# Performance work log

Hardware: AMD Instinct MI355X
Metric: run time of the kernel (lower is better)

## Reference

```python
import jax, jax.numpy as jnp
import numpy as np

K = 5          # number of spline bins
B = 5.0        # tail bound
HIDDEN = 8
MIN_W = 1e-3; MIN_H = 1e-3; MIN_D = 1e-3  # RQS defaults (Durkan et al.)


def setup_inputs() -> dict:
    n, d = 32768, 64
    L = d - 1
    P = 3 * K - 1
    ks = jax.random.split(jax.random.key(0), 8)
    x = jax.random.normal(ks[0], (n, d), jnp.float32) * 2.0
    init_param = jax.random.uniform(ks[1], (P,), jnp.float32, -0.5, 0.5)
    # ragged first layers: layer l (predicts dim l+1) sees x[:, :l+1]; zero-pad to width L
    mask = (jnp.arange(L)[None, :] <= jnp.arange(L)[:, None]).astype(jnp.float32)
    W1 = jax.random.normal(ks[2], (L, L, HIDDEN), jnp.float32) * 0.2 * mask[:, :, None]
    b1 = jax.random.normal(ks[3], (L, HIDDEN), jnp.float32) * 0.1
    W2 = jax.random.normal(ks[4], (L, HIDDEN, HIDDEN), jnp.float32) * 0.2
    b2 = jax.random.normal(ks[5], (L, HIDDEN), jnp.float32) * 0.1
    W3 = jax.random.normal(ks[6], (L, HIDDEN, P), jnp.float32) * 0.2
    b3 = jax.random.normal(ks[7], (L, P), jnp.float32) * 0.1
    return {"x": x, "init_param": init_param, "W1": W1, "b1": b1,
            "W2": W2, "b2": b2, "W3": W3, "b3": b3}


def _rqs(xf, Wu, Hu, Du):
    # xf: (M,), Wu/Hu: (M,K), Du: (M,K-1) -- vectorized unconstrained RQS, forward
    inside = (xf >= -B) & (xf <= B)
    const = float(np.log(np.exp(1.0 - MIN_D) - 1.0))
    Dpad = jnp.pad(Du, ((0, 0), (1, 1)), constant_values=const)

    widths = MIN_W + (1.0 - MIN_W * K) * jax.nn.softmax(Wu, axis=-1)
    cumw = jnp.pad(jnp.cumsum(widths, -1), ((0, 0), (1, 0)))
    cumw = 2.0 * B * cumw - B
    cumw = cumw.at[:, 0].set(-B).at[:, -1].set(B)
    widths = cumw[:, 1:] - cumw[:, :-1]

    heights = MIN_H + (1.0 - MIN_H * K) * jax.nn.softmax(Hu, axis=-1)
    cumh = jnp.pad(jnp.cumsum(heights, -1), ((0, 0), (1, 0)))
    cumh = 2.0 * B * cumh - B
    cumh = cumh.at[:, 0].set(-B).at[:, -1].set(B)
    heights = cumh[:, 1:] - cumh[:, :-1]

    derivs = MIN_D + jax.nn.softplus(Dpad)  # (M, K+1)

    xc = jnp.clip(xf, -B, B)
    idx = jnp.clip(jnp.sum(xc[:, None] >= cumw, axis=-1) - 1, 0, K - 1)
    take = lambda a: jnp.take_along_axis(a, idx[:, None], axis=-1)[:, 0]

    icw, ibw = take(cumw), take(widths)
    ich, ih = take(cumh), take(heights)
    idl = take(heights / widths)
    idv = take(derivs)
    idvp1 = take(derivs[:, 1:])

    theta = (xc - icw) / ibw
    tmt = theta * (1.0 - theta)
    num = ih * (idl * theta * theta + idv * tmt)
    den = idl + (idv + idvp1 - 2.0 * idl) * tmt
    out = ich + num / den
    dnum = idl * idl * (idvp1 * theta * theta + 2.0 * idl * tmt + idv * (1.0 - theta) ** 2)
    ld = jnp.log(dnum) - 2.0 * jnp.log(den)
    return jnp.where(inside, out, xf), jnp.where(inside, ld, 0.0)


def reference(x, init_param, W1, b1, W2, b2, W3, b3):
    n, d = x.shape
    L = d - 1
    P = 3 * K - 1
    # mask re-applied so padded W1 entries are exactly inert (ragged Linear(i, hidden))
    mask = (jnp.arange(L)[None, :] <= jnp.arange(L)[:, None]).astype(x.dtype)
    h = jnp.tanh(jnp.einsum('nj,ljh->lnh', x[:, :L], W1 * mask[:, :, None]) + b1[:, None, :])
    h = jnp.tanh(jnp.einsum('lnh,lhg->lng', h, W2) + b2[:, None, :])
    out = jnp.einsum('lng,lgp->lnp', h, W3) + b3[:, None, :]      # (L, n, P)
    p0 = jnp.broadcast_to(init_param, (1, n, P))                  # dim 0 uses init_param
    params = jnp.concatenate([p0, out], axis=0).reshape(d * n, P)  # dim-major, matches Ws layout
    Wu, Hu, Du = params[:, :K], params[:, K:2 * K], params[:, 2 * K:]
    xf = x.T.reshape(-1)  # x.transpose(0,1).flatten()
    zs, lds = _rqs(xf, Wu, Hu, Du)
    # NOTE: faithfully replicates the original's reshape of the dim-major flat
    # vector directly to (n, d) (as in the torch source).
    return zs.reshape(n, d), lds.reshape(n, d).sum(axis=1)
```

## Files before the change

### kernel.cpp

```cpp
#include <hip/hip_runtime.h>
#include <hip/hip_bf16.h>
#include <math.h>

#define KK 5
#define Bc 5.0f
#define NN 32768
#define DD 64
#define LL 63
#define PP 14
#define MIN_Wc 0.001f
#define MIN_Hc 0.001f
#define MIN_Dc 0.001f

typedef float f4 __attribute__((ext_vector_type(4)));
typedef float f32x4 __attribute__((ext_vector_type(4)));
typedef float f2 __attribute__((ext_vector_type(2)));
typedef short short8 __attribute__((ext_vector_type(8)));

__device__ __forceinline__ float rcp_fast(float v)  { return __builtin_amdgcn_rcpf(v); }
__device__ __forceinline__ float exp_fast(float v)  { return __expf(v); }
__device__ __forceinline__ float log_fast(float v)  { return __logf(v); }
__device__ __forceinline__ float tanh_fast(float v) {
    float e = exp_fast(2.0f * v);
    return 1.0f - 2.0f * rcp_fast(e + 1.0f);
}
__device__ __forceinline__ float softplus_fast(float v) {
    return (v > 15.0f) ? v : log_fast(1.0f + exp_fast(v));
}
__device__ __forceinline__ ushort to_bf16u(float v) {
    __hip_bfloat16 b = __float2bfloat16(v);
    return *(ushort*)&b;
}
__device__ __forceinline__ f2 splat2(float v) { f2 r; r.x = v; r.y = v; return r; }
__device__ __forceinline__ f4 splat4(float v) { f4 r; r.x = v; r.y = v; r.z = v; r.w = v; return r; }

__global__ __launch_bounds__(256) void pack_b1(const float* __restrict__ W1,
                                               ushort* __restrict__ Bp) {
    int id = blockIdx.x * 256 + threadIdx.x;
    int n = id >> 6, k = id & 63;
    float v = 0.f;
    if (n < 504 && k < 63) {
        int l = n >> 3, h = n & 7;
        v = W1[(l * 63 + k) * 8 + h];
    }
    Bp[id] = to_bf16u(v);
}

__device__ __forceinline__ short8 pack_a(f4 v0, f4 v1) {
    short8 a;
    a[0] = (short)to_bf16u(v0.x); a[1] = (short)to_bf16u(v0.y);
    a[2] = (short)to_bf16u(v0.z); a[3] = (short)to_bf16u(v0.w);
    a[4] = (short)to_bf16u(v1.x); a[5] = (short)to_bf16u(v1.y);
    a[6] = (short)to_bf16u(v1.z); a[7] = (short)to_bf16u(v1.w);
    return a;
}

#define WSL 216

__device__ __forceinline__ void do_dim(
    int dd, const float* wp, float xf, uint4 hv, int s0, int lane, int bx,
    const float* __restrict__ init_param, float* __restrict__ out)
{
    float p0,p1,p2,p3,p4,p5,p6,p7,p8,p9,p10,p11,p12,p13;
    if (dd == 0) {
        p0 = init_param[0];  p1 = init_param[1];  p2 = init_param[2];
        p3 = init_param[3];  p4 = init_param[4];  p5 = init_param[5];
        p6 = init_param[6];  p7 = init_param[7];  p8 = init_param[8];
        p9 = init_param[9];  p10 = init_param[10]; p11 = init_param[11];
        p12 = init_param[12]; p13 = init_param[13];
    } else {
        float h1f[8];
        h1f[0] = __uint_as_float(hv.x << 16);
        h1f[1] = __uint_as_float(hv.x & 0xFFFF0000u);
        h1f[2] = __uint_as_float(hv.y << 16);
        h1f[3] = __uint_as_float(hv.y & 0xFFFF0000u);
        h1f[4] = __uint_as_float(hv.z << 16);
        h1f[5] = __uint_as_float(hv.z & 0xFFFF0000u);
        h1f[6] = __uint_as_float(hv.w << 16);
        h1f[7] = __uint_as_float(hv.w & 0xFFFF0000u);

        f4 h2a = *(const f4*)(wp + 64);
        f4 h2b = *(const f4*)(wp + 68);
        #pragma unroll
        for (int h = 0; h < 8; ++h) {
            f4 wa = *(const f4*)(wp + h * 8);
            f4 wb = *(const f4*)(wp + h * 8 + 4);
            f4 av = splat4(h1f[h]);
            h2a += av * wa;
            h2b += av * wb;
        }
        float h2f[8];
        h2f[0] = tanh_fast(h2a.x); h2f[1] = tanh_fast(h2a.y);
        h2f[2] = tanh_fast(h2a.z); h2f[3] = tanh_fast(h2a.w);
        h2f[4] = tanh_fast(h2b.x); h2f[5] = tanh_fast(h2b.y);
        h2f[6] = tanh_fast(h2b.z); h2f[7] = tanh_fast(h2b.w);

        f4 ppa = *(const f4*)(wp + 200);
        f4 ppb = *(const f4*)(wp + 204);
        f4 ppc = *(const f4*)(wp + 208);
        f4 ppd = *(const f4*)(wp + 212);
        #pragma unroll
        for (int g = 0; g < 8; ++g) {
            const float* wr = wp + 72 + g * 16;
            f4 w0 = *(const f4*)(wr);
            f4 w1 = *(const f4*)(wr + 4);
            f4 w2v = *(const f4*)(wr + 8);
            f4 w3v = *(const f4*)(wr + 12);
            f4 av = splat4(h2f[g]);
            ppa += av * w0;
            ppb += av * w1;
            ppc += av * w2v;
            ppd += av * w3v;
        }
        p0 = ppa.x; p1 = ppa.y; p2 = ppa.z; p3 = ppa.w;
        p4 = ppb.x; p5 = ppb.y; p6 = ppb.z; p7 = ppb.w;
        p8 = ppc.x; p9 = ppc.y; p10 = ppc.z; p11 = ppc.w;
        p12 = ppd.x; p13 = ppd.y;
    }

    f2 e0, e1, e2, e3, e4;
    e0.x = exp_fast(p0); e0.y = exp_fast(p5);
    e1.x = exp_fast(p1); e1.y = exp_fast(p6);
    e2.x = exp_fast(p2); e2.y = exp_fast(p7);
    e3.x = exp_fast(p3); e3.y = exp_fast(p8);
    e4.x = exp_fast(p4); e4.y = exp_fast(p9);
    f2 es = e0 + e1 + e2 + e3 + e4;
    f2 nrm; nrm.x = 0.995f * rcp_fast(es.x); nrm.y = 0.995f * rcp_fast(es.y);

    const f2 minv = {MIN_Wc, MIN_Hc};
    f2 cb0 = splat2(-Bc), acc2 = splat2(0.f);
    acc2 += minv + nrm * e0;  f2 cb1 = splat2(2.f * Bc) * acc2 - splat2(Bc);
    acc2 += minv + nrm * e1;  f2 cb2 = splat2(2.f * Bc) * acc2 - splat2(Bc);
    acc2 += minv + nrm * e2;  f2 cb3 = splat2(2.f * Bc) * acc2 - splat2(Bc);
    acc2 += minv + nrm * e3;  f2 cb4 = splat2(2.f * Bc) * acc2 - splat2(Bc);
    f2 cb5 = splat2(Bc);

    const float xc = fminf(fmaxf(xf, -Bc), Bc);

    float icw = cb0.x, ich = cb0.y;
    float ibw = cb1.x - cb0.x, ih = cb1.y - cb0.y;
    float rv = p10, rvp = p10;
    bool v_one = true, vp_one = false;
    {
        bool c = xc >= cb1.x; f2 dif = cb2 - cb1;
        icw = c ? cb1.x : icw; ich = c ? cb1.y : ich;
        ibw = c ? dif.x : ibw; ih  = c ? dif.y : ih;
        v_one = c ? false : v_one; rv = c ? p10 : rv; rvp = c ? p11 : rvp;
    }
    {
        bool c = xc >= cb2.x; f2 dif = cb3 - cb2;
        icw = c ? cb2.x : icw; ich = c ? cb2.y : ich;
        ibw = c ? dif.x : ibw; ih  = c ? dif.y : ih;
        rv = c ? p11 : rv; rvp = c ? p12 : rvp;
    }
    {
        bool c = xc >= cb3.x; f2 dif = cb4 - cb3;
        icw = c ? cb3.x : icw; ich = c ? cb3.y : ich;
        ibw = c ? dif.x : ibw; ih  = c ? dif.y : ih;
        rv = c ? p12 : rv; rvp = c ? p13 : rvp;
    }
    {
        bool c = xc >= cb4.x; f2 dif = cb5 - cb4;
        icw = c ? cb4.x : icw; ich = c ? cb4.y : ich;
        ibw = c ? dif.x : ibw; ih  = c ? dif.y : ih;
        rv = c ? p13 : rv; vp_one = c;
    }
    const float idv   = v_one  ? 1.0f : MIN_Dc + softplus_fast(rv);
    const float idvp1 = vp_one ? 1.0f : MIN_Dc + softplus_fast(rvp);

    const float ibw_r = rcp_fast(ibw);
    const float idl = ih * ibw_r;
    const float theta = (xc - icw) * ibw_r;
    const float omt = 1.0f - theta;
    const float tmt = theta * omt;
    const float num = ih * (idl * theta * theta + idv * tmt);
    const float den = idl + (idv + idvp1 - 2.0f * idl) * tmt;
    const float dr = rcp_fast(den);
    const float outv = ich + num * dr;
    const float dnum = idl * idl * (idvp1 * theta * theta + 2.0f * idl * tmt + idv * omt * omt);
    const float ld = log_fast(dnum * dr * dr);

    const bool inside = (xf >= -Bc) && (xf <= Bc);
    const float z = inside ? outv : xf;
    float ldv = inside ? ld : 0.0f;

    out[dd * NN + s0 + lane] = z;

    #pragma unroll
    for (int off = 32; off > 0; off >>= 1) ldv += __shfl_down(ldv, off);
    if (lane == 0) out[NN * DD + dd * (NN / 64) + bx] = ldv;
}

#define H1S 136
__global__ __launch_bounds__(256, 5) void fused_kernel(
    const float* __restrict__ x, const float* __restrict__ init_param,
    const ushort* __restrict__ Bp, const float* __restrict__ b1,
    const float* __restrict__ W2, const float* __restrict__ b2,
    const float* __restrict__ W3, const float* __restrict__ b3,
    float* __restrict__ out)
{
    __shared__ ushort h1c[64 * H1S];
    __shared__ float  wl[16 * WSL];
    const int tid = threadIdx.x;
    const int s0 = blockIdx.x * 64;
    const int y  = blockIdx.y;
    const int bx = blockIdx.x;
    const int lane = tid & 63;
    const int wave = __builtin_amdgcn_readfirstlane(tid >> 6);
    const int ln = lane & 15, qg = lane >> 4;
    const int m0 = wave * 16;
    const int l0 = y * 16;

    const float* xrow = x + (size_t)(s0 + lane) * 64;
    const int db = y * 16 + 1 + wave * 4;
    float xv0 = xrow[db];
    float xv1 = xrow[db + 1];
    float xv2 = xrow[db + 2];
    float xv3 = xrow[(y == 3 && wave == 3) ? 0 : db + 3];

    short8 a0, a1;
    {
        const float* xr = x + (size_t)(s0 + m0 + ln) * 64 + qg * 8;
        a0 = pack_a(*(const f4*)xr, *(const f4*)(xr + 4));
        a1 = (y >= 2) ? pack_a(*(const f4*)(xr + 32), *(const f4*)(xr + 36)) : a0;
    }

    {
        int s = tid >> 4, o = (tid & 15) * 4;
        if (l0 + s < LL)
            *(f4*)&wl[s * WSL + o] = *(const f4*)&W2[(l0 + s) * 64 + o];
    }
    if (tid < 128) {
        int s = tid >> 3, o = tid & 7;
        if (l0 + s < LL) wl[s * WSL + 64 + o] = b2[(l0 + s) * 8 + o];
    }
    #pragma unroll
    for (int q0 = 0; q0 < 896; q0 += 256) {
        int q = q0 + tid;
        if (q < 896) {
            int s = q / 56, r = q % 56, g = r / 7, o = r % 7;
            *(f2*)&wl[s * WSL + 72 + g * 16 + o * 2] =
                *(const f2*)&W3[(l0 + s) * 112 + g * 14 + o * 2];
        }
    }
    if (tid < 128) {
        int s = tid >> 3, g = tid & 7;
        *(f2*)&wl[s * WSL + 72 + g * 16 + 14] = splat2(0.f);
    }
    if (tid < 224) {
        int s = tid / 14, o = tid % 14;
        wl[s * WSL + 200 + o] = b3[(l0 + s < LL ? l0 + s : 0) * PP + o];
    }
    if (tid < 32) {
        int s = tid >> 1, o = 214 + (tid & 1);
        wl[s * WSL + o] = 0.f;
    }

    #pragma unroll
    for (int nt = 0; nt < 8; ++nt) {
        int ncol = y * 128 + nt * 16 + ln;
        const short8* bp8 = (const short8*)(Bp + ncol * 64 + qg * 8);
        f32x4 acc = {0.f, 0.f, 0.f, 0.f};
        acc = __builtin_amdgcn_mfma_f32_16x16x32_bf16(a0, bp8[0], acc, 0, 0, 0);
        if (y >= 2)
            acc = __builtin_amdgcn_mfma_f32_16x16x32_bf16(a1, bp8[4], acc, 0, 0, 0);
        float bias = (ncol < 504) ? b1[ncol] : 0.f;
        #pragma unroll
        for (int r = 0; r < 4; ++r) {
            float v = tanh_fast(acc[r] + bias);
            h1c[(m0 + qg * 4 + r) * H1S + nt * 16 + ln] = to_bf16u(v);
        }
    }
    __syncthreads();

    const uint4* hp = (const uint4*)&h1c[lane * H1S + wave * 32];
    uint4 hv0 = hp[0], hv1 = hp[1], hv2 = hp[2], hv3 = hp[3];

    const int sl = wave * 4;
    do_dim(db,     wl + (sl)     * WSL, xv0, hv0, s0, lane, bx, init_param, out);
    do_dim(db + 1, wl + (sl + 1) * WSL, xv1, hv1, s0, lane, bx, init_param, out);
    do_dim(db + 2, wl + (sl + 2) * WSL, xv2, hv2, s0, lane, bx, init_param, out);
    do_dim((y == 3 && wave == 3) ? 0 : db + 3,
                   wl + (sl + 3) * WSL, xv3, hv3, s0, lane, bx, init_param, out);
}

extern "C" void kernel_launch(void* const* d_in, const int* in_sizes, int n_in,
                              void* d_out, int out_size, void* d_ws, size_t ws_size,
                              hipStream_t stream) {
    const float* x          = (const float*)d_in[0];
    const float* init_param = (const float*)d_in[1];
    const float* W1         = (const float*)d_in[2];
    const float* b1         = (const float*)d_in[3];
    const float* W2         = (const float*)d_in[4];
    const float* b2         = (const float*)d_in[5];
    const float* W3         = (const float*)d_in[6];
    const float* b3         = (const float*)d_in[7];
    float* out = (float*)d_out;

    ushort* Bp = (ushort*)d_ws;

    pack_b1<<<128, 256, 0, stream>>>(W1, Bp);
    fused_kernel<<<dim3(512, 4), 256, 0, stream>>>(x, init_param, Bp, b1,
                                                   W2, b2, W3, b3, out);
}
```

Baseline: 111.1 us.

## Retile fused kernel to 128 samples x 8 dims per block with paired processing

Reorganises the grid so each block handles 128 samples and 8 output dims instead of 64 samples and 16 dims. Each wave now processes two sample rows per dim, which reuses the MFMA B fragments and the LDS weights across both rows and gives more independent work for instruction-level parallelism. The factor of 2 inside tanh is folded into the pre-scaled W2/b2 and b1 so the tanh path skips a multiply. In exchange the kernel uses more registers (launch bounds drop to 4 waves per SIMD) and the log-det partial sums are indexed differently.

```diff
diff --git a/kernel.cpp b/kernel.cpp
--- a/kernel.cpp
+++ b/kernel.cpp
@@ -20,8 +20,8 @@
 __device__ __forceinline__ float rcp_fast(float v)  { return __builtin_amdgcn_rcpf(v); }
 __device__ __forceinline__ float exp_fast(float v)  { return __expf(v); }
 __device__ __forceinline__ float log_fast(float v)  { return __logf(v); }
-__device__ __forceinline__ float tanh_fast(float v) {
-    float e = exp_fast(2.0f * v);
+__device__ __forceinline__ float tanh_pre(float t2) {
+    float e = exp_fast(t2);
     return 1.0f - 2.0f * rcp_fast(e + 1.0f);
 }
 __device__ __forceinline__ float softplus_fast(float v) {
@@ -56,232 +56,282 @@
 }
 
 #define WSL 216
-
-__device__ __forceinline__ void do_dim(
-    int dd, const float* wp, float xf, uint4 hv, int s0, int lane, int bx,
-    const float* __restrict__ init_param, float* __restrict__ out)
+#define H1S 72
+
+__device__ __forceinline__ void do_dim2(
+    int dd, const float* wp, float xf0, float xf1, uint4 hv0, uint4 hv1,
+    int s0, int lane, int bx,
+    const float* __restrict__ ip, float* __restrict__ out)
 {
-    float p0,p1,p2,p3,p4,p5,p6,p7,p8,p9,p10,p11,p12,p13;
-    if (dd == 0) {
-        p0 = init_param[0];  p1 = init_param[1];  p2 = init_param[2];
-        p3 = init_param[3];  p4 = init_param[4];  p5 = init_param[5];
-        p6 = init_param[6];  p7 = init_param[7];  p8 = init_param[8];
-        p9 = init_param[9];  p10 = init_param[10]; p11 = init_param[11];
-        p12 = init_param[12]; p13 = init_param[13];
-    } else {
-        float h1f[8];
-        h1f[0] = __uint_as_float(hv.x << 16);
-        h1f[1] = __uint_as_float(hv.x & 0xFFFF0000u);
-        h1f[2] = __uint_as_float(hv.y << 16);
-        h1f[3] = __uint_as_float(hv.y & 0xFFFF0000u);
-        h1f[4] = __uint_as_float(hv.z << 16);
-        h1f[5] = __uint_as_float(hv.z & 0xFFFF0000u);
-        h1f[6] = __uint_as_float(hv.w << 16);
-        h1f[7] = __uint_as_float(hv.w & 0xFFFF0000u);
-
-        f4 h2a = *(const f4*)(wp + 64);
-        f4 h2b = *(const f4*)(wp + 68);
+    float p0a[PP], p1a[PP];
+    {
+        float h0[8], h1[8];
+        h0[0] = __uint_as_float(hv0.x << 16);         h1[0] = __uint_as_float(hv1.x << 16);
+        h0[1] = __uint_as_float(hv0.x & 0xFFFF0000u); h1[1] = __uint_as_float(hv1.x & 0xFFFF0000u);
+        h0[2] = __uint_as_float(hv0.y << 16);         h1[2] = __uint_as_float(hv1.y << 16);
+        h0[3] = __uint_as_float(hv0.y & 0xFFFF0000u); h1[3] = __uint_as_float(hv1.y & 0xFFFF0000u);
+        h0[4] = __uint_as_float(hv0.z << 16);         h1[4] = __uint_as_float(hv1.z << 16);
+        h0[5] = __uint_as_float(hv0.z & 0xFFFF0000u); h1[5] = __uint_as_float(hv1.z & 0xFFFF0000u);
+        h0[6] = __uint_as_float(hv0.w << 16);         h1[6] = __uint_as_float(hv1.w << 16);
+        h0[7] = __uint_as_float(hv0.w & 0xFFFF0000u); h1[7] = __uint_as_float(hv1.w & 0xFFFF0000u);
+
+        f4 a0 = *(const f4*)(wp + 64), b0 = *(const f4*)(wp + 68);
+        f4 a1 = a0, b1 = b0;
         #pragma unroll
         for (int h = 0; h < 8; ++h) {
             f4 wa = *(const f4*)(wp + h * 8);
             f4 wb = *(const f4*)(wp + h * 8 + 4);
-            f4 av = splat4(h1f[h]);
-            h2a += av * wa;
-            h2b += av * wb;
-        }
-        float h2f[8];
-        h2f[0] = tanh_fast(h2a.x); h2f[1] = tanh_fast(h2a.y);
-        h2f[2] = tanh_fast(h2a.z); h2f[3] = tanh_fast(h2a.w);
-        h2f[4] = tanh_fast(h2b.x); h2f[5] = tanh_fast(h2b.y);
-        h2f[6] = tanh_fast(h2b.z); h2f[7] = tanh_fast(h2b.w);
-
-        f4 ppa = *(const f4*)(wp + 200);
-        f4 ppb = *(const f4*)(wp + 204);
-        f4 ppc = *(const f4*)(wp + 208);
-        f4 ppd = *(const f4*)(wp + 212);
+            f4 av0 = splat4(h0[h]), av1 = splat4(h1[h]);
+            a0 += av0 * wa;  a1 += av1 * wa;
+            b0 += av0 * wb;  b1 += av1 * wb;
+        }
+        float g0[8], g1[8];
+        g0[0] = tanh_pre(a0.x); g1[0] = tanh_pre(a1.x);
+        g0[1] = tanh_pre(a0.y); g1[1] = tanh_pre(a1.y);
+        g0[2] = tanh_pre(a0.z); g1[2] = tanh_pre(a1.z);
+        g0[3] = tanh_pre(a0.w); g1[3] = tanh_pre(a1.w);
+        g0[4] = tanh_pre(b0.x); g1[4] = tanh_pre(b1.x);
+        g0[5] = tanh_pre(b0.y); g1[5] = tanh_pre(b1.y);
+        g0[6] = tanh_pre(b0.z); g1[6] = tanh_pre(b1.z);
+        g0[7] = tanh_pre(b0.w); g1[7] = tanh_pre(b1.w);
+
+        f4 pa0 = *(const f4*)(wp + 200), pb0 = *(const f4*)(wp + 204);
+        f4 pc0 = *(const f4*)(wp + 208), pd0 = *(const f4*)(wp + 212);
+        f4 pa1 = pa0, pb1 = pb0, pc1 = pc0, pd1 = pd0;
         #pragma unroll
         for (int g = 0; g < 8; ++g) {
             const float* wr = wp + 72 + g * 16;
             f4 w0 = *(const f4*)(wr);
             f4 w1 = *(const f4*)(wr + 4);
-            f4 w2v = *(const f4*)(wr + 8);
-            f4 w3v = *(const f4*)(wr + 12);
-            f4 av = splat4(h2f[g]);
-            ppa += av * w0;
-            ppb += av * w1;
-            ppc += av * w2v;
-            ppd += av * w3v;
-        }
-        p0 = ppa.x; p1 = ppa.y; p2 = ppa.z; p3 = ppa.w;
-        p4 = ppb.x; p5 = ppb.y; p6 = ppb.z; p7 = ppb.w;
-        p8 = ppc.x; p9 = ppc.y; p10 = ppc.z; p11 = ppc.w;
-        p12 = ppd.x; p13 = ppd.y;
-    }
-
-    f2 e0, e1, e2, e3, e4;
-    e0.x = exp_fast(p0); e0.y = exp_fast(p5);
-    e1.x = exp_fast(p1); e1.y = exp_fast(p6);
-    e2.x = exp_fast(p2); e2.y = exp_fast(p7);
-    e3.x = exp_fast(p3); e3.y = exp_fast(p8);
-    e4.x = exp_fast(p4); e4.y = exp_fast(p9);
-    f2 es = e0 + e1 + e2 + e3 + e4;
-    f2 nrm; nrm.x = 0.995f * rcp_fast(es.x); nrm.y = 0.995f * rcp_fast(es.y);
-
-    const f2 minv = {MIN_Wc, MIN_Hc};
-    f2 cb0 = splat2(-Bc), acc2 = splat2(0.f);
-    acc2 += minv + nrm * e0;  f2 cb1 = splat2(2.f * Bc) * acc2 - splat2(Bc);
-    acc2 += minv + nrm * e1;  f2 cb2 = splat2(2.f * Bc) * acc2 - splat2(Bc);
-    acc2 += minv + nrm * e2;  f2 cb3 = splat2(2.f * Bc) * acc2 - splat2(Bc);
-    acc2 += minv + nrm * e3;  f2 cb4 = splat2(2.f * Bc) * acc2 - splat2(Bc);
-    f2 cb5 = splat2(Bc);
-
-    const float xc = fminf(fmaxf(xf, -Bc), Bc);
-
-    float icw = cb0.x, ich = cb0.y;
-    float ibw = cb1.x - cb0.x, ih = cb1.y - cb0.y;
-    float rv = p10, rvp = p10;
-    bool v_one = true, vp_one = false;
-    {
-        bool c = xc >= cb1.x; f2 dif = cb2 - cb1;
-        icw = c ? cb1.x : icw; ich = c ? cb1.y : ich;
-        ibw = c ? dif.x : ibw; ih  = c ? dif.y : ih;
-        v_one = c ? false : v_one; rv = c ? p10 : rv; rvp = c ? p11 : rvp;
-    }
-    {
-        bool c = xc >= cb2.x; f2 dif = cb3 - cb2;
-        icw = c ? cb2.x : icw; ich = c ? cb2.y : ich;
-        ibw = c ? dif.x : ibw; ih  = c ? dif.y : ih;
-        rv = c ? p11 : rv; rvp = c ? p12 : rvp;
-    }
-    {
-        bool c = xc >= cb3.x; f2 dif = cb4 - cb3;
-        icw = c ? cb3.x : icw; ich = c ? cb3.y : ich;
-        ibw = c ? dif.x : ibw; ih  = c ? dif.y : ih;
-        rv = c ? p12 : rv; rvp = c ? p13 : rvp;
-    }
-    {
-        bool c = xc >= cb4.x; f2 dif = cb5 - cb4;
-        icw = c ? cb4.x : icw; ich = c ? cb4.y : ich;
-        ibw = c ? dif.x : ibw; ih  = c ? dif.y : ih;
-        rv = c ? p13 : rv; vp_one = c;
-    }
-    const float idv   = v_one  ? 1.0f : MIN_Dc + softplus_fast(rv);
-    const float idvp1 = vp_one ? 1.0f : MIN_Dc + softplus_fast(rvp);
-
-    const float ibw_r = rcp_fast(ibw);
-    const float idl = ih * ibw_r;
-    const float theta = (xc - icw) * ibw_r;
-    const float omt = 1.0f - theta;
-    const float tmt = theta * omt;
-    const float num = ih * (idl * theta * theta + idv * tmt);
-    const float den = idl + (idv + idvp1 - 2.0f * idl) * tmt;
-    const float dr = rcp_fast(den);
-    const float outv = ich + num * dr;
-    const float dnum = idl * idl * (idvp1 * theta * theta + 2.0f * idl * tmt + idv * omt * omt);
-    const float ld = log_fast(dnum * dr * dr);
-
-    const bool inside = (xf >= -Bc) && (xf <= Bc);
-    const float z = inside ? outv : xf;
-    float ldv = inside ? ld : 0.0f;
-
-    out[dd * NN + s0 + lane] = z;
+            f4 w2 = *(const f4*)(wr + 8);
+            f4 w3 = *(const f4*)(wr + 12);
+            f4 av0 = splat4(g0[g]), av1 = splat4(g1[g]);
+            pa0 += av0 * w0;  pa1 += av1 * w0;
+            pb0 += av0 * w1;  pb1 += av1 * w1;
+            pc0 += av0 * w2;  pc1 += av1 * w2;
+            pd0 += av0 * w3;  pd1 += av1 * w3;
+        }
+        p0a[0]=pa0.x; p0a[1]=pa0.y; p0a[2]=pa0.z; p0a[3]=pa0.w;
+        p0a[4]=pb0.x; p0a[5]=pb0.y; p0a[6]=pb0.z; p0a[7]=pb0.w;
+        p0a[8]=pc0.x; p0a[9]=pc0.y; p0a[10]=pc0.z; p0a[11]=pc0.w;
+        p0a[12]=pd0.x; p0a[13]=pd0.y;
+        p1a[0]=pa1.x; p1a[1]=pa1.y; p1a[2]=pa1.z; p1a[3]=pa1.w;
+        p1a[4]=pb1.x; p1a[5]=pb1.y; p1a[6]=pb1.z; p1a[7]=pb1.w;
+        p1a[8]=pc1.x; p1a[9]=pc1.y; p1a[10]=pc1.z; p1a[11]=pc1.w;
+        p1a[12]=pd1.x; p1a[13]=pd1.y;
+    }
+
+    if (dd == 0) {
+        #pragma unroll
+        for (int i = 0; i < PP; ++i) { p0a[i] = ip[i]; p1a[i] = ip[i]; }
+    }
+
+    f4 e0, e1, e2, e3, e4;
+    e0.x = exp_fast(p0a[0]); e0.y = exp_fast(p0a[5]); e0.z = exp_fast(p1a[0]); e0.w = exp_fast(p1a[5]);
+    e1.x = exp_fast(p0a[1]); e1.y = exp_fast(p0a[6]); e1.z = exp_fast(p1a[1]); e1.w = exp_fast(p1a[6]);
+    e2.x = exp_fast(p0a[2]); e2.y = exp_fast(p0a[7]); e2.z = exp_fast(p1a[2]); e2.w = exp_fast(p1a[7]);
+    e3.x = exp_fast(p0a[3]); e3.y = exp_fast(p0a[8]); e3.z = exp_fast(p1a[3]); e3.w = exp_fast(p1a[8]);
+    e4.x = exp_fast(p0a[4]); e4.y = exp_fast(p0a[9]); e4.z = exp_fast(p1a[4]); e4.w = exp_fast(p1a[9]);
+    f4 es = (e0 + e1) + (e2 + e3) + e4;
+    f4 nrm;
+    nrm.x = 0.995f * rcp_fast(es.x); nrm.y = 0.995f * rcp_fast(es.y);
+    nrm.z = 0.995f * rcp_fast(es.z); nrm.w = 0.995f * rcp_fast(es.w);
+
+    const f4 minv = {MIN_Wc, MIN_Hc, MIN_Wc, MIN_Hc};
+    f4 acc4 = splat4(0.f);
+    acc4 += minv + nrm * e0;  f4 cb1 = splat4(2.f * Bc) * acc4 - splat4(Bc);
+    acc4 += minv + nrm * e1;  f4 cb2 = splat4(2.f * Bc) * acc4 - splat4(Bc);
+    acc4 += minv + nrm * e2;  f4 cb3 = splat4(2.f * Bc) * acc4 - splat4(Bc);
+    acc4 += minv + nrm * e3;  f4 cb4 = splat4(2.f * Bc) * acc4 - splat4(Bc);
+
+    const float xc0 = fminf(fmaxf(xf0, -Bc), Bc);
+    const float xc1 = fminf(fmaxf(xf1, -Bc), Bc);
+
+    float icw0 = -Bc, ich0 = -Bc, ibw0 = cb1.x + Bc, ih0 = cb1.y + Bc;
+    float icw1 = -Bc, ich1 = -Bc, ibw1 = cb1.z + Bc, ih1 = cb1.w + Bc;
+    float rv0 = p0a[10], rvp0 = p0a[10], rv1 = p1a[10], rvp1 = p1a[10];
+    bool vone0 = true, vpone0 = false, vone1 = true, vpone1 = false;
+    {
+        bool c0 = xc0 >= cb1.x;               bool c1 = xc1 >= cb1.z;
+        icw0 = c0 ? cb1.x : icw0;             icw1 = c1 ? cb1.z : icw1;
+        ich0 = c0 ? cb1.y : ich0;             ich1 = c1 ? cb1.w : ich1;
+        ibw0 = c0 ? cb2.x - cb1.x : ibw0;     ibw1 = c1 ? cb2.z - cb1.z : ibw1;
+        ih0  = c0 ? cb2.y - cb1.y : ih0;      ih1  = c1 ? cb2.w - cb1.w : ih1;
+        vone0 = c0 ? false : vone0;           vone1 = c1 ? false : vone1;
+        rv0  = c0 ? p0a[10] : rv0;            rv1  = c1 ? p1a[10] : rv1;
+        rvp0 = c0 ? p0a[11] : rvp0;           rvp1 = c1 ? p1a[11] : rvp1;
+    }
+    {
+        bool c0 = xc0 >= cb2.x;               bool c1 = xc1 >= cb2.z;
+        icw0 = c0 ? cb2.x : icw0;             icw1 = c1 ? cb2.z : icw1;
+        ich0 = c0 ? cb2.y : ich0;             ich1 = c1 ? cb2.w : ich1;
+        ibw0 = c0 ? cb3.x - cb2.x : ibw0;     ibw1 = c1 ? cb3.z - cb2.z : ibw1;
+        ih0  = c0 ? cb3.y - cb2.y : ih0;      ih1  = c1 ? cb3.w - cb2.w : ih1;
+        rv0  = c0 ? p0a[11] : rv0;            rv1  = c1 ? p1a[11] : rv1;
+        rvp0 = c0 ? p0a[12] : rvp0;           rvp1 = c1 ? p1a[12] : rvp1;
+    }
+    {
+        bool c0 = xc0 >= cb3.x;               bool c1 = xc1 >= cb3.z;
+        icw0 = c0 ? cb3.x : icw0;             icw1 = c1 ? cb3.z : icw1;
+        ich0 = c0 ? cb3.y : ich0;             ich1 = c1 ? cb3.w : ich1;
+        ibw0 = c0 ? cb4.x - cb3.x : ibw0;     ibw1 = c1 ? cb4.z - cb3.z : ibw1;
+        ih0  = c0 ? cb4.y - cb3.y : ih0;      ih1  = c1 ? cb4.w - cb3.w : ih1;
+        rv0  = c0 ? p0a[12] : rv0;            rv1  = c1 ? p1a[12] : rv1;
+        rvp0 = c0 ? p0a[13] : rvp0;           rvp1 = c1 ? p1a[13] : rvp1;
+    }
+    {
+        bool c0 = xc0 >= cb4.x;               bool c1 = xc1 >= cb4.z;
+        icw0 = c0 ? cb4.x : icw0;             icw1 = c1 ? cb4.z : icw1;
+        ich0 = c0 ? cb4.y : ich0;             ich1 = c1 ? cb4.w : ich1;
+        ibw0 = c0 ? Bc - cb4.x : ibw0;        ibw1 = c1 ? Bc - cb4.z : ibw1;
+        ih0  = c0 ? Bc - cb4.y : ih0;         ih1  = c1 ? Bc - cb4.w : ih1;
+        rv0  = c0 ? p0a[13] : rv0;            rv1  = c1 ? p1a[13] : rv1;
+        vpone0 = c0;                          vpone1 = c1;
+    }
+    const float idv0   = vone0  ? 1.0f : MIN_Dc + softplus_fast(rv0);
+    const float idv1   = vone1  ? 1.0f : MIN_Dc + softplus_fast(rv1);
+    const float idvp0  = vpone0 ? 1.0f : MIN_Dc + softplus_fast(rvp0);
+    const float idvp1_ = vpone1 ? 1.0f : MIN_Dc + softplus_fast(rvp1);
+
+    const float ibr0 = rcp_fast(ibw0);        const float ibr1 = rcp_fast(ibw1);
+    const float idl0 = ih0 * ibr0;            const float idl1 = ih1 * ibr1;
+    const float th0 = (xc0 - icw0) * ibr0;    const float th1 = (xc1 - icw1) * ibr1;
+    const float om0 = 1.0f - th0;             const float om1 = 1.0f - th1;
+    const float tm0 = th0 * om0;              const float tm1 = th1 * om1;
+    const float num0 = ih0 * (idl0 * th0 * th0 + idv0 * tm0);
+    const float num1 = ih1 * (idl1 * th1 * th1 + idv1 * tm1);
+    const float den0 = idl0 + (idv0 + idvp0 - 2.0f * idl0) * tm0;
+    const float den1 = idl1 + (idv1 + idvp1_ - 2.0f * idl1) * tm1;
+    const float dr0 = rcp_fast(den0);         const float dr1 = rcp_fast(den1);
+    const float out0 = ich0 + num0 * dr0;     const float out1v = ich1 + num1 * dr1;
+    const float dn0 = idl0 * idl0 * (idvp0 * th0 * th0 + 2.0f * idl0 * tm0 + idv0 * om0 * om0);
+    const float dn1 = idl1 * idl1 * (idvp1_ * th1 * th1 + 2.0f * idl1 * tm1 + idv1 * om1 * om1);
+    const float ld0 = log_fast(dn0 * dr0 * dr0);
+    const float ld1 = log_fast(dn1 * dr1 * dr1);
+
+    const bool in0 = (xf0 >= -Bc) && (xf0 <= Bc);
+    const bool in1 = (xf1 >= -Bc) && (xf1 <= Bc);
+    const float z0 = in0 ? out0 : xf0;        const float z1 = in1 ? out1v : xf1;
+    float lv0 = in0 ? ld0 : 0.0f;             float lv1 = in1 ? ld1 : 0.0f;
+
+    out[dd * NN + s0 + lane] = z0;
+    out[dd * NN + s0 + 64 + lane] = z1;
 
     #pragma unroll
-    for (int off = 32; off > 0; off >>= 1) ldv += __shfl_down(ldv, off);
-    if (lane == 0) out[NN * DD + dd * (NN / 64) + bx] = ldv;
-}
-
-#define H1S 136
-__global__ __launch_bounds__(256, 5) void fused_kernel(
+    for (int off = 32; off > 0; off >>= 1) {
+        lv0 += __shfl_down(lv0, off);
+        lv1 += __shfl_down(lv1, off);
+    }
+    if (lane == 0) {
+        out[NN * DD + dd * (NN / 64) + 2 * bx]     = lv0;
+        out[NN * DD + dd * (NN / 64) + 2 * bx + 1] = lv1;
+    }
+}
+
+__global__ __launch_bounds__(256, 4) void fused_kernel(
     const float* __restrict__ x, const float* __restrict__ init_param,
     const ushort* __restrict__ Bp, const float* __restrict__ b1,
     const float* __restrict__ W2, const float* __restrict__ b2,
     const float* __restrict__ W3, const float* __restrict__ b3,
     float* __restrict__ out)
 {
-    __shared__ ushort h1c[64 * H1S];
-    __shared__ float  wl[16 * WSL];
+    __shared__ ushort h1c[128 * H1S];
+    __shared__ float  wl[8 * WSL];
     const int tid = threadIdx.x;
-    const int s0 = blockIdx.x * 64;
+    const int s0 = blockIdx.x * 128;
     const int y  = blockIdx.y;
     const int bx = blockIdx.x;
     const int lane = tid & 63;
     const int wave = __builtin_amdgcn_readfirstlane(tid >> 6);
     const int ln = lane & 15, qg = lane >> 4;
-    const int m0 = wave * 16;
-    const int l0 = y * 16;
-
-    const float* xrow = x + (size_t)(s0 + lane) * 64;
-    const int db = y * 16 + 1 + wave * 4;
-    float xv0 = xrow[db];
-    float xv1 = xrow[db + 1];
-    float xv2 = xrow[db + 2];
-    float xv3 = xrow[(y == 3 && wave == 3) ? 0 : db + 3];
-
-    short8 a0, a1;
-    {
-        const float* xr = x + (size_t)(s0 + m0 + ln) * 64 + qg * 8;
-        a0 = pack_a(*(const f4*)xr, *(const f4*)(xr + 4));
-        a1 = (y >= 2) ? pack_a(*(const f4*)(xr + 32), *(const f4*)(xr + 36)) : a0;
-    }
-
-    {
+    const int l0 = y * 8;
+
+    const int dA = y * 8 + 1 + 2 * wave;
+    const int dB_raw = dA + 1;
+    const int dB = (y == 7 && wave == 3) ? 0 : dB_raw;
+    const float* xr0 = x + (size_t)(s0 + lane) * 64;
+    const float* xr1 = xr0 + 64 * 64;
+    float xA0 = xr0[dA], xA1 = xr1[dA];
+    float xB0 = xr0[dB], xB1 = xr1[dB];
+
+    short8 a0_0, a1_0, a0_1, a1_1;
+    {
+        const float* p0 = x + (size_t)(s0 + wave * 16 + ln) * 64 + qg * 8;
+        const float* p1 = p0 + 64 * 64;
+        a0_0 = pack_a(*(const f4*)p0, *(const f4*)(p0 + 4));
+        a0_1 = pack_a(*(const f4*)p1, *(const f4*)(p1 + 4));
+        if (y >= 4) {
+            a1_0 = pack_a(*(const f4*)(p0 + 32), *(const f4*)(p0 + 36));
+            a1_1 = pack_a(*(const f4*)(p1 + 32), *(const f4*)(p1 + 36));
+        } else { a1_0 = a0_0; a1_1 = a0_1; }
+    }
+
+    if (tid < 128) {
         int s = tid >> 4, o = (tid & 15) * 4;
         if (l0 + s < LL)
-            *(f4*)&wl[s * WSL + o] = *(const f4*)&W2[(l0 + s) * 64 + o];
-    }
-    if (tid < 128) {
+            *(f4*)&wl[s * WSL + o] = splat4(2.f) * (*(const f4*)&W2[(l0 + s) * 64 + o]);
+    }
+    if (tid < 64) {
         int s = tid >> 3, o = tid & 7;
-        if (l0 + s < LL) wl[s * WSL + 64 + o] = b2[(l0 + s) * 8 + o];
+        if (l0 + s < LL) wl[s * WSL + 64 + o] = 2.f * b2[(l0 + s) * 8 + o];
     }
     #pragma unroll
-    for (int q0 = 0; q0 < 896; q0 += 256) {
+    for (int q0 = 0; q0 < 448; q0 += 256) {
         int q = q0 + tid;
-        if (q < 896) {
+        if (q < 448) {
             int s = q / 56, r = q % 56, g = r / 7, o = r % 7;
-            *(f2*)&wl[s * WSL + 72 + g * 16 + o * 2] =
-                *(const f2*)&W3[(l0 + s) * 112 + g * 14 + o * 2];
-        }
-    }
-    if (tid < 128) {
+            if (l0 + s < LL)
+                *(f2*)&wl[s * WSL + 72 + g * 16 + o * 2] =
+                    *(const f2*)&W3[(l0 + s) * 112 + g * 14 + o * 2];
+        }
+    }
+    if (tid < 64) {
         int s = tid >> 3, g = tid & 7;
         *(f2*)&wl[s * WSL + 72 + g * 16 + 14] = splat2(0.f);
     }
-    if (tid < 224) {
+    if (tid < 112) {
         int s = tid / 14, o = tid % 14;
         wl[s * WSL + 200 + o] = b3[(l0 + s < LL ? l0 + s : 0) * PP + o];
     }
-    if (tid < 32) {
+    if (tid < 16) {
         int s = tid >> 1, o = 214 + (tid & 1);
         wl[s * WSL + o] = 0.f;
     }
 
     #pragma unroll
-    for (int nt = 0; nt < 8; ++nt) {
-        int ncol = y * 128 + nt * 16 + ln;
+    for (int nt = 0; nt < 4; ++nt) {
+        int ncol = y * 64 + nt * 16 + ln;
         const short8* bp8 = (const short8*)(Bp + ncol * 64 + qg * 8);
-        f32x4 acc = {0.f, 0.f, 0.f, 0.f};
-        acc = __builtin_amdgcn_mfma_f32_16x16x32_bf16(a0, bp8[0], acc, 0, 0, 0);
-        if (y >= 2)
-            acc = __builtin_amdgcn_mfma_f32_16x16x32_bf16(a1, bp8[4], acc, 0, 0, 0);
-        float bias = (ncol < 504) ? b1[ncol] : 0.f;
+        short8 bf0 = bp8[0];
+        f32x4 acc0 = {0.f, 0.f, 0.f, 0.f};
+        f32x4 acc1 = {0.f, 0.f, 0.f, 0.f};
+        acc0 = __builtin_amdgcn_mfma_f32_16x16x32_bf16(a0_0, bf0, acc0, 0, 0, 0);
+        acc1 = __builtin_amdgcn_mfma_f32_16x16x32_bf16(a0_1, bf0, acc1, 0, 0, 0);
+        if (y >= 4) {
+            short8 bf1 = bp8[4];
+            acc0 = __builtin_amdgcn_mfma_f32_16x16x32_bf16(a1_0, bf1, acc0, 0, 0, 0);
+            acc1 = __builtin_amdgcn_mfma_f32_16x16x32_bf16(a1_1, bf1, acc1, 0, 0, 0);
+        }
+        float bias2 = (ncol < 504) ? 2.f * b1[ncol] : 0.f;
         #pragma unroll
         for (int r = 0; r < 4; ++r) {
-            float v = tanh_fast(acc[r] + bias);
-            h1c[(m0 + qg * 4 + r) * H1S + nt * 16 + ln] = to_bf16u(v);
+            int row = wave * 16 + qg * 4 + r;
+            float v0 = tanh_pre(fmaf(2.0f, acc0[r], bias2));
+            float v1 = tanh_pre(fmaf(2.0f, acc1[r], bias2));
+            h1c[row * H1S + nt * 16 + ln] = to_bf16u(v0);
+            h1c[(row + 64) * H1S + nt * 16 + ln] = to_bf16u(v1);
         }
     }
     __syncthreads();
 
-    const uint4* hp = (const uint4*)&h1c[lane * H1S + wave * 32];
-    uint4 hv0 = hp[0], hv1 = hp[1], hv2 = hp[2], hv3 = hp[3];
-
-    const int sl = wave * 4;
-    do_dim(db,     wl + (sl)     * WSL, xv0, hv0, s0, lane, bx, init_param, out);
-    do_dim(db + 1, wl + (sl + 1) * WSL, xv1, hv1, s0, lane, bx, init_param, out);
-    do_dim(db + 2, wl + (sl + 2) * WSL, xv2, hv2, s0, lane, bx, init_param, out);
-    do_dim((y == 3 && wave == 3) ? 0 : db + 3,
-                   wl + (sl + 3) * WSL, xv3, hv3, s0, lane, bx, init_param, out);
+    const int slA = 2 * wave, slB = 2 * wave + 1;
+    uint4 hA0 = *(const uint4*)&h1c[lane * H1S + slA * 8];
+    uint4 hA1 = *(const uint4*)&h1c[(lane + 64) * H1S + slA * 8];
+    uint4 hB0 = *(const uint4*)&h1c[lane * H1S + slB * 8];
+    uint4 hB1 = *(const uint4*)&h1c[(lane + 64) * H1S + slB * 8];
+
+    do_dim2(dA, wl + slA * WSL, xA0, xA1, hA0, hA1, s0, lane, bx, init_param, out);
+    do_dim2(dB, wl + slB * WSL, xB0, xB1, hB0, hB1, s0, lane, bx, init_param, out);
 }
 
 extern "C" void kernel_launch(void* const* d_in, const int* in_sizes, int n_in,
@@ -300,6 +350,6 @@
     ushort* Bp = (ushort*)d_ws;
 
     pack_b1<<<128, 256, 0, stream>>>(W1, Bp);
-    fused_kernel<<<dim3(512, 4), 256, 0, stream>>>(x, init_param, Bp, b1,
+    fused_kernel<<<dim3(256, 8), 256, 0, stream>>>(x, init_param, Bp, b1,
                                                    W2, b2, W3, b3, out);
 }
```

After: 177.9 us. 1.6x slower.
